# Kernel tuning notes

Hardware: AMD Instinct MI355X
Metric: run time of the kernel (lower is better)

Reference implementation:

```python
import jax, jax.numpy as jnp
import numpy as np

R = 6            # search radius
P = 2 * R + 1    # patch size = 13
D = 4            # mask downsample rate
TOPK = 36        # top-k over patch dim (eval path)


def _corr(fq, fm):
    """Local correlation volume (SpatialCorrelationSampler, kernel=1, patch=P).
    fq, fm: [b,c,h,w] -> [b, P*P, h*w]."""
    b, c, h, w = fq.shape
    fmp = jnp.pad(fm, ((0, 0), (0, 0), (R, R), (R, R)))
    rows = []
    for di in range(P):
        for dj in range(P):
            rows.append(jnp.einsum('bchw,bchw->bhw', fq, fmp[:, :, di:di + h, dj:dj + w]))
    return jnp.stack(rows, 1).reshape(b, P * P, h * w)


def _unfold(msk):
    """F.unfold(msk, kernel_size=P, padding=R): [b,o,h,w] -> [b,o,P*P,h*w]."""
    b, o, h, w = msk.shape
    mp = jnp.pad(msk, ((0, 0), (0, 0), (R, R), (R, R)))
    pats = [mp[:, :, di:di + h, dj:dj + w] for di in range(P) for dj in range(P)]
    return jnp.stack(pats, 2).reshape(b, o, P * P, h * w)


def _forward(feat_query, feat_mem0, feat_mem1, msk_mem0, msk_mem1):
    b, c, h, w = feat_query.shape
    # correlation volumes for each memory frame, concat over patch dim
    corr = jnp.concatenate([_corr(feat_query, feat_mem0),
                            _corr(feat_query, feat_mem1)], axis=1)
    corr = corr / jnp.sqrt(jnp.asarray(c, corr.dtype))          # [b, 2*P*P, N]
    # eval path: top-k over the (frames*P*P) patch axis, per pixel
    corr_t = corr.transpose(0, 2, 1)                              # [b, N, 2PP]
    vals, idx = jax.lax.top_k(corr_t, TOPK)                       # [b, N, K]
    wts = jax.nn.softmax(vals, axis=-1)                           # [b, N, K]
    # downsample masks by strided slicing, unfold, concat over patch dim
    msk = jnp.concatenate([_unfold(msk_mem0[:, :, ::D, ::D]),
                           _unfold(msk_mem1[:, :, ::D, ::D])], axis=2)  # [b,o,2PP,N]
    msk_t = msk.transpose(0, 3, 1, 2)                             # [b, N, o, 2PP]
    g = jnp.take_along_axis(msk_t, idx[:, :, None, :], axis=3)    # [b, N, o, K]
    out = (wts[:, :, None, :] * g).sum(-1)                        # [b, N, o]
    obj = msk_mem0.shape[1]
    return out.transpose(0, 2, 1).reshape(b, obj, h, w)


def setup_inputs() -> dict:
    key = jax.random.key(0)
    k = jax.random.split(key, 5)
    b, c, h, w = 1, 256, 120, 216
    obj = 11
    return {
        'feat_query': jax.random.normal(k[0], (b, c, h, w), jnp.float32),
        'feat_mem0': jax.random.normal(k[1], (b, c, h, w), jnp.float32),
        'feat_mem1': jax.random.normal(k[2], (b, c, h, w), jnp.float32),
        'msk_mem0': jax.random.uniform(k[3], (b, obj, h * D, w * D), jnp.float32),
        'msk_mem1': jax.random.uniform(k[4], (b, obj, h * D, w * D), jnp.float32),
    }


def reference(feat_query, feat_mem0, feat_mem1, msk_mem0, msk_mem1):
    return _forward(feat_query, feat_mem0, feat_mem1, msk_mem0, msk_mem1)
```

## Files before the change

kernel.cpp:

```cpp
#include <hip/hip_runtime.h>
#include <hip/hip_bf16.h>
#include <math.h>

#define H 120
#define W 216
#define C 256
#define NPIX (H*W)
#define PATCH 13
#define PP 169
#define RAD 6
#define TOPKN 36
#define OBJ 11
#define MD 4
#define CW 344

typedef unsigned short ushort;
typedef unsigned int   uint;
typedef __attribute__((ext_vector_type(8))) __bf16 bf16x8;
typedef __attribute__((ext_vector_type(4))) float   f32x4;

#define PLANE_B ((size_t)NPIX * 512)

#define YT 8
#define RT 20
#define XT 16
#define UW 32
#define PXS 128
#define ROWS (UW * PXS)
#define BUFB (RT * ROWS)
#define NXT 14
#define NYT 15
#define NWG (NXT * 2 * NYT)

__device__ inline ushort f2bf_rne(float x) {
  uint u = __float_as_uint(x);
  uint r = (u + 0x7FFFu + ((u >> 16) & 1u)) >> 16;
  return (ushort)r;
}
__device__ inline float bf2f(ushort h) { return __uint_as_float(((uint)h) << 16); }

__global__ __launch_bounds__(256) void k_prep(const float* __restrict__ fq,
                      const float* __restrict__ fm0, const float* __restrict__ fm1,
                      char* fqt, char* fm0t, char* fm1t) {
  const float* src = (blockIdx.z == 0) ? fq : (blockIdx.z == 1) ? fm0 : fm1;
  char* dst = (blockIdx.z == 0) ? fqt : (blockIdx.z == 1) ? fm0t : fm1t;

  const int p0 = blockIdx.x * 64;
  const int c0 = blockIdx.y * 64;
  const int tid = threadIdx.x;

  __shared__ float ts[64 * 65];
  {
    int p = tid & 63, cl = tid >> 6;
    #pragma unroll
    for (int jj = 0; jj < 16; ++jj) {
      int c = 4 * jj + cl;
      ts[c * 65 + p] = src[(size_t)(c0 + c) * NPIX + p0 + p];
    }
  }
  __syncthreads();
  {
    int pl = tid >> 2, sub = tid & 3;
    ushort hb[16], lb[16];
    #pragma unroll
    for (int i = 0; i < 16; ++i) {
      float x = ts[(sub * 16 + i) * 65 + pl];
      ushort h = f2bf_rne(x);
      hb[i] = h;
      lb[i] = f2bf_rne(x - bf2f(h));
    }
    size_t off = (size_t)(p0 + pl) * 512 + (size_t)c0 * 2 + sub * 32;
    *(uint4*)(dst + off)            = ((uint4*)hb)[0];
    *(uint4*)(dst + off + 16)       = ((uint4*)hb)[1];
    *(uint4*)(dst + PLANE_B + off)      = ((uint4*)lb)[0];
    *(uint4*)(dst + PLANE_B + off + 16) = ((uint4*)lb)[1];
  }
}

__global__ void k_downsample(const float* __restrict__ m0, const float* __restrict__ m1,
                             float* __restrict__ mds) {
  int i = blockIdx.x * 256 + threadIdx.x;
  const int total = 2 * OBJ * NPIX;
  if (i >= total) return;
  int fo = i / NPIX;
  int pix = i - fo * NPIX;
  int f = fo / OBJ, o = fo - f * OBJ;
  int y = pix / W, x = pix - y * W;
  const float* src = f ? m1 : m0;
  mds[i] = src[(size_t)o * (H*MD) * (W*MD) + (size_t)(MD*y) * (W*MD) + MD*x];
}

__global__ __launch_bounds__(512, 2) void k_corr_mfma(const char* __restrict__ fqt,
                        const char* __restrict__ fm0t, const char* __restrict__ fm1t,
                        float* __restrict__ corr) {
  int b = blockIdx.x;
  int xcd = b & 7;
  int wgid = ((xcd < 4) ? xcd * 53 : 4 * 53 + (xcd - 4) * 52) + (b >> 3);
  int yt   = wgid % NYT;
  int rest = wgid / NYT;
  int f    = rest & 1;
  int xt   = rest >> 1;

  const int y0 = yt * YT;
  const int X0 = xt * XT;
  const int tid  = threadIdx.x;
  const int wy   = tid >> 6;
  const int lane = tid & 63;
  const int l15  = lane & 15, l4 = lane >> 4;
  const int y    = y0 + wy;

  const char* frame = f ? fm1t : fm0t;

  __shared__ __align__(16) char bsm[2 * BUFB];

  const char* gsrc[10];
  #pragma unroll
  for (int i = 0; i < 10; ++i) {
    int gdest = wy * 640 + i * 64 + lane;
    int ri  = gdest >> 8;
    int rem = gdest & 255;
    int px  = rem >> 3;
    int pqp = rem & 7;
    int pqs = pqp ^ (px & 7);
    int p   = pqs >> 2, q = pqs & 3;
    int r = y0 - 6 + ri;  r = (r < 0) ? 0 : (r >= H ? H - 1 : r);
    int u = X0 - 8 + px;  u = (u < 0) ? 0 : (u >= W ? W - 1 : u);
    gsrc[i] = frame + (size_t)p * PLANE_B + (size_t)(r * W + u) * 512 + q * 16;
  }

  int xA = X0 + l15;
  const char* pa = fqt + (size_t)(y * W + (xA < W ? xA : W - 1)) * 512 + l4 * 16;
  bf16x8 Ah[8], Al[8];
  #pragma unroll
  for (int kc = 0; kc < 8; ++kc) {
    Ah[kc] = *(const bf16x8*)(pa + kc * 64);
    Al[kc] = *(const bf16x8*)(pa + PLANE_B + kc * 64);
  }

  const int px0 = l15, px1 = 16 + l15;
  const uint sw  = (uint)((l15 & 7) << 4);
  const uint b0h = (uint)((px0 * PXS +      l4 * 16) ^ sw);
  const uint b0l = (uint)((px0 * PXS + 64 + l4 * 16) ^ sw);
  const uint b1h = (uint)((px1 * PXS +      l4 * 16) ^ sw);
  const uint b1l = (uint)((px1 * PXS + 64 + l4 * 16) ^ sw);

  int u0 = X0 + l15 - 8;
  int u1 = u0 + 16;
  bool uok0 = (u0 >= 0) && (u0 < W);
  bool uok1 = (u1 >= 0) && (u1 < W);

  f32x4 acc[13][2];
  #pragma unroll
  for (int di = 0; di < 13; ++di) {
    acc[di][0] = (f32x4){0.f, 0.f, 0.f, 0.f};
    acc[di][1] = (f32x4){0.f, 0.f, 0.f, 0.f};
  }

  auto STAGE = [&](int buf, int kc) {
    #pragma unroll
    for (int i = 0; i < 10; ++i)
      __builtin_amdgcn_global_load_lds(
        (const __attribute__((address_space(1))) void*)(gsrc[i] + kc * 64),
        (__attribute__((address_space(3))) void*)(bsm + buf * BUFB + wy * 10240 + i * 1024),
        16, 0, 0);
  };

  STAGE(0, 0);
  __syncthreads();

  #pragma unroll
  for (int kc = 0; kc < 8; ++kc) {
    if (kc < 7) STAGE((kc + 1) & 1, kc + 1);
    const char* bb = bsm + (kc & 1) * BUFB;

    #pragma unroll
    for (int di = 0; di < 13; ++di) {
      int rr = y + di - RAD;
      if (rr >= 0 && rr < H) {
        const char* rb = bb + (wy + di) * ROWS;
        {
          bf16x8 Bhv = *(const bf16x8*)(rb + b0h);
          bf16x8 Blv = *(const bf16x8*)(rb + b0l);
          acc[di][0] = __builtin_amdgcn_mfma_f32_16x16x32_bf16(Ah[kc], Bhv, acc[di][0], 0, 0, 0);
          acc[di][0] = __builtin_amdgcn_mfma_f32_16x16x32_bf16(Ah[kc], Blv, acc[di][0], 0, 0, 0);
          acc[di][0] = __builtin_amdgcn_mfma_f32_16x16x32_bf16(Al[kc], Bhv, acc[di][0], 0, 0, 0);
        }
        {
          bf16x8 Bhv = *(const bf16x8*)(rb + b1h);
          bf16x8 Blv = *(const bf16x8*)(rb + b1l);
          acc[di][1] = __builtin_amdgcn_mfma_f32_16x16x32_bf16(Ah[kc], Bhv, acc[di][1], 0, 0, 0);
          acc[di][1] = __builtin_amdgcn_mfma_f32_16x16x32_bf16(Ah[kc], Blv, acc[di][1], 0, 0, 0);
          acc[di][1] = __builtin_amdgcn_mfma_f32_16x16x32_bf16(Al[kc], Bhv, acc[di][1], 0, 0, 0);
        }
      }
    }
    __syncthreads();
  }

  float* cb = corr + (size_t)(y * W) * CW + f * PP;
  #pragma unroll
  for (int di = 0; di < 13; ++di) {
    #pragma unroll
    for (int nt = 0; nt < 2; ++nt) {
      bool uok = nt ? uok1 : uok0;
      #pragma unroll
      for (int j = 0; j < 4; ++j) {
        int m  = l4 * 4 + j;
        int x  = X0 + m;
        int dj = 16 * nt + l15 - m - 2;
        if (x < W && dj >= 0 && dj < PATCH)
          cb[(size_t)x * CW + di * PATCH + dj] = uok ? acc[di][nt][j] * 0.0625f : 0.f;
      }
    }
  }
}

__global__ __launch_bounds__(64) void k_corr_valu(const float* __restrict__ fq,
                       const float* __restrict__ fm0, const float* __restrict__ fm1,
                       float* __restrict__ corr) {
  int b = blockIdx.x;
  int lb = (b & 7) * 390 + (b >> 3);
  int y   = lb / 26;
  int r26 = lb - y * 26;
  int f   = r26 / 13;
  int di  = r26 - f * 13;
  const int tid = threadIdx.x;
  const int xg  = tid;
  const int r   = y + di - RAD;

  float* corr_base = corr + (size_t)(y * W) * CW + (f * PP + di * PATCH);

  if (r < 0 || r >= H) {
    if (xg < 54) {
      float* cp = corr_base + (size_t)(4 * xg) * CW;
      #pragma unroll
      for (int sub = 0; sub < 4; ++sub) {
        #pragma unroll
        for (int dj = 0; dj < PATCH; ++dj) cp[(size_t)sub * CW + dj] = 0.f;
      }
    }
    return;
  }

  const float* fm = f ? fm1 : fm0;
  __shared__ float fm_s[4 * 232];

  const float* pf[4];
  int  ldsoff[4];
  bool sval[4], mval[4];
  #pragma unroll
  for (int s = 0; s < 4; ++s) {
    int i = tid + 64 * s;
    sval[s] = (i < 232);
    int ii = sval[s] ? i : 0;
    int ch = ii / 58;
    int m  = ii - ch * 58;
    int x  = 4 * m - 8;
    mval[s] = sval[s] && (m >= 2) && (m <= 55);
    ldsoff[s] = ch * 232 + 4 * m;
    pf[s] = fm + (size_t)ch * NPIX + (size_t)r * W + (mval[s] ? x : 0);
  }

  const float* pq = fq + (size_t)y * W + 4 * ((xg < 54) ? xg : 0);

  float4 acc[PATCH];
  #pragma unroll
  for (int d = 0; d < PATCH; ++d) acc[d] = make_float4(0.f, 0.f, 0.f, 0.f);

  for (int c0 = 0; c0 < C; c0 += 4) {
    #pragma unroll
    for (int s = 0; s < 4; ++s) {
      if (sval[s]) {
        float4 v = make_float4(0.f, 0.f, 0.f, 0.f);
        if (mval[s]) v = *(const float4*)(pf[s]);
        *(float4*)&fm_s[ldsoff[s]] = v;
        pf[s] += 4 * (size_t)NPIX;
      }
    }
    __syncthreads();
    if (xg < 54) {
      #pragma unroll
      for (int ch = 0; ch < 4; ++ch) {
        float4 q4 = *(const float4*)(pq + (size_t)ch * NPIX);
        float rv[20];
        #pragma unroll
        for (int qq = 0; qq < 5; ++qq) {
          float4 t4 = *(const float4*)&fm_s[ch * 232 + 4 * xg + 4 * qq];
          rv[4*qq+0] = t4.x; rv[4*qq+1] = t4.y; rv[4*qq+2] = t4.z; rv[4*qq+3] = t4.w;
        }
        #pragma unroll
        for (int dj = 0; dj < PATCH; ++dj) {
          acc[dj].x += q4.x * rv[dj + 2];
          acc[dj].y += q4.y * rv[dj + 3];
          acc[dj].z += q4.z * rv[dj + 4];
          acc[dj].w += q4.w * rv[dj + 5];
        }
      }
      pq += 4 * (size_t)NPIX;
    }
    __syncthreads();
  }

  if (xg < 54) {
    float* cp = corr_base + (size_t)(4 * xg) * CW;
    #pragma unroll
    for (int dj = 0; dj < PATCH; ++dj) {
      cp[dj]                  = acc[dj].x * 0.0625f;
      cp[(size_t)1 * CW + dj] = acc[dj].y * 0.0625f;
      cp[(size_t)2 * CW + dj] = acc[dj].z * 0.0625f;
      cp[(size_t)3 * CW + dj] = acc[dj].w * 0.0625f;
    }
  }
}

__global__ __launch_bounds__(256) void k_topk(const float* __restrict__ corr,
                       const float* __restrict__ mds, float* __restrict__ out) {
  int wid = (blockIdx.x * 256 + threadIdx.x) >> 6;
  int lane = threadIdx.x & 63;
  if (wid >= NPIX) return;
  const float* cr = corr + (size_t)wid * CW;

  float v[6]; uint ui[6];
  #pragma unroll
  for (int s = 0; s < 6; ++s) {
    int idx = lane + 64 * s;
    bool ok = idx < 2 * PP;
    float f = ok ? cr[idx] : 0.f;
    v[s] = f;
    uint bb = __float_as_uint(f);
    uint u = bb ^ (uint)(((int)bb >> 31) | 0x80000000);
    ui[s] = ok ? u : 0u;
  }

  uint blo = 0u, bhi = 0xFFFFFFFFu;
  for (int it = 0; it < 32; ++it) {
    uint mid = blo + ((bhi - blo) >> 1);
    int c = 0;
    #pragma unroll
    for (int s = 0; s < 6; ++s)
      c += __popcll(__ballot(ui[s] > mid));
    if (c <= 35) bhi = mid; else blo = mid + 1;
  }
  const uint x0 = blo;

  int c_gt = 0;
  #pragma unroll
  for (int s = 0; s < 6; ++s) c_gt += __popcll(__ballot(ui[s] > x0));
  const int need = 36 - c_gt;

  uint tb = (x0 & 0x80000000u) ? (x0 ^ 0x80000000u) : ~x0;
  const float tf = __uint_as_float(tb);

  float w[6];
  float zp = 0.f;
  int prior = 0;
  #pragma unroll
  for (int s = 0; s < 6; ++s) {
    unsigned long long tie = __ballot(ui[s] == x0);
    uint below = __builtin_amdgcn_mbcnt_hi((uint)(tie >> 32),
                  __builtin_amdgcn_mbcnt_lo((uint)tie, 0u));
    bool acc = (ui[s] > x0) || ((ui[s] == x0) && ((prior + (int)below) < need));
    prior += __popcll(tie);
    w[s] = acc ? __expf(v[s] - tf) : 0.f;
    zp += w[s];
  }
  float Z = zp;
  #pragma unroll
  for (int off = 32; off >= 1; off >>= 1) Z += __shfl_xor(Z, off, 64);

  int y = wid / W, x = wid - (wid / W) * W;
  float no[OBJ];
  #pragma unroll
  for (int o = 0; o < OBJ; ++o) no[o] = 0.f;
  #pragma unroll
  for (int s = 0; s < 6; ++s) {
    if (w[s] > 0.f) {
      int idx = lane + 64 * s;
      int ff = idx >= PP;
      int r = idx - ff * PP;
      int di = r / PATCH, dj = r - (r / PATCH) * PATCH;
      int yy = y + di - RAD, xx = x + dj - RAD;
      if (yy >= 0 && yy < H && xx >= 0 && xx < W) {
        const float* mb = mds + ((size_t)ff * OBJ) * NPIX + yy * W + xx;
        #pragma unroll
        for (int o = 0; o < OBJ; ++o) no[o] += w[s] * mb[(size_t)o * NPIX];
      }
    }
  }
  float inv = 1.f / Z;
  #pragma unroll
  for (int o = 0; o < OBJ; ++o) {
    float p = no[o];
    #pragma unroll
    for (int off = 32; off >= 1; off >>= 1) p += __shfl_xor(p, off, 64);
    if (lane == 0) out[(size_t)o * NPIX + wid] = p * inv;
  }
}

extern "C" void kernel_launch(void* const* d_in, const int* in_sizes, int n_in,
                              void* d_out, int out_size, void* d_ws, size_t ws_size,
                              hipStream_t stream) {
  const float* fq  = (const float*)d_in[0];
  const float* fm0 = (const float*)d_in[1];
  const float* fm1 = (const float*)d_in[2];
  const float* m0  = (const float*)d_in[3];
  const float* m1  = (const float*)d_in[4];
  float* out = (float*)d_out;

  char* ws = (char*)d_ws;
  size_t off = 0;
  auto alloc = [&](size_t sz) { size_t o = off; off = (off + sz + 1023) & ~(size_t)1023; return o; };

  size_t mds_o  = alloc((size_t)2 * OBJ * NPIX * sizeof(float));
  size_t corr_o = alloc((size_t)NPIX * CW * sizeof(float));
  size_t fqt_o  = alloc(2 * PLANE_B);
  size_t fm0t_o = alloc(2 * PLANE_B);
  size_t fm1t_o = alloc(2 * PLANE_B);
  size_t needed = off;

  float* mds  = (float*)(ws + mds_o);
  float* corr = (float*)(ws + corr_o);

  k_downsample<<<(2 * OBJ * NPIX + 255) / 256, 256, 0, stream>>>(m0, m1, mds);

  if (ws_size >= needed) {
    char* fqt  = ws + fqt_o;
    char* fm0t = ws + fm0t_o;
    char* fm1t = ws + fm1t_o;
    dim3 gp(405, 4, 3);
    k_prep<<<gp, 256, 0, stream>>>(fq, fm0, fm1, fqt, fm0t, fm1t);
    k_corr_mfma<<<NWG, 512, 0, stream>>>(fqt, fm0t, fm1t, corr);
  } else {
    k_corr_valu<<<120 * 26, 64, 0, stream>>>(fq, fm0, fm1, corr);
  }

  k_topk<<<NPIX / 4, 256, 0, stream>>>(corr, mds, out);
}
```

Baseline: 138.5 us.

## Split MFMA corr work across twice the waves and stream A fragments per k-chunk

The correlation kernel now runs 1024 threads per block, with each wave handling a single 16-pixel column tile instead of two. This halves the accumulator registers per wave. The query A fragments are no longer all preloaded; they are loaded per k-chunk with a one-step-ahead prefetch. The aim is to cut VGPR pressure and raise the number of resident waves, so LDS reads and MFMA latency overlap better. In exchange, each wave issues more duplicated A loads, LDS B reads are no longer shared across the two column tiles, and the launch-bounds target of 1024x4 may cause spilling.

```diff
diff --git a/kernel.cpp b/kernel.cpp
--- a/kernel.cpp
+++ b/kernel.cpp
@@ -90,7 +90,7 @@
   mds[i] = src[(size_t)o * (H*MD) * (W*MD) + (size_t)(MD*y) * (W*MD) + MD*x];
 }
 
-__global__ __launch_bounds__(512, 2) void k_corr_mfma(const char* __restrict__ fqt,
+__global__ __launch_bounds__(1024, 4) void k_corr_mfma(const char* __restrict__ fqt,
                         const char* __restrict__ fm0t, const char* __restrict__ fm1t,
                         float* __restrict__ corr) {
   int b = blockIdx.x;
@@ -104,19 +104,21 @@
   const int y0 = yt * YT;
   const int X0 = xt * XT;
   const int tid  = threadIdx.x;
-  const int wy   = tid >> 6;
+  const int wv   = tid >> 6;
+  const int wyy  = wv >> 1;
+  const int nt   = wv & 1;
   const int lane = tid & 63;
   const int l15  = lane & 15, l4 = lane >> 4;
-  const int y    = y0 + wy;
+  const int y    = y0 + wyy;
 
   const char* frame = f ? fm1t : fm0t;
 
   __shared__ __align__(16) char bsm[2 * BUFB];
 
-  const char* gsrc[10];
-  #pragma unroll
-  for (int i = 0; i < 10; ++i) {
-    int gdest = wy * 640 + i * 64 + lane;
+  const char* gsrc[5];
+  #pragma unroll
+  for (int i = 0; i < 5; ++i) {
+    int gdest = wv * 64 + lane + 1024 * i;
     int ri  = gdest >> 8;
     int rem = gdest & 255;
     int px  = rem >> 3;
@@ -130,70 +132,58 @@
 
   int xA = X0 + l15;
   const char* pa = fqt + (size_t)(y * W + (xA < W ? xA : W - 1)) * 512 + l4 * 16;
-  bf16x8 Ah[8], Al[8];
-  #pragma unroll
-  for (int kc = 0; kc < 8; ++kc) {
-    Ah[kc] = *(const bf16x8*)(pa + kc * 64);
-    Al[kc] = *(const bf16x8*)(pa + PLANE_B + kc * 64);
-  }
-
-  const int px0 = l15, px1 = 16 + l15;
+
+  const int pxn = 16 * nt + l15;
   const uint sw  = (uint)((l15 & 7) << 4);
-  const uint b0h = (uint)((px0 * PXS +      l4 * 16) ^ sw);
-  const uint b0l = (uint)((px0 * PXS + 64 + l4 * 16) ^ sw);
-  const uint b1h = (uint)((px1 * PXS +      l4 * 16) ^ sw);
-  const uint b1l = (uint)((px1 * PXS + 64 + l4 * 16) ^ sw);
-
-  int u0 = X0 + l15 - 8;
-  int u1 = u0 + 16;
-  bool uok0 = (u0 >= 0) && (u0 < W);
-  bool uok1 = (u1 >= 0) && (u1 < W);
-
-  f32x4 acc[13][2];
-  #pragma unroll
-  for (int di = 0; di < 13; ++di) {
-    acc[di][0] = (f32x4){0.f, 0.f, 0.f, 0.f};
-    acc[di][1] = (f32x4){0.f, 0.f, 0.f, 0.f};
-  }
+  const uint bh_off = (uint)((pxn * PXS +      l4 * 16) ^ sw);
+  const uint bl_off = (uint)((pxn * PXS + 64 + l4 * 16) ^ sw);
+
+  int u0 = X0 + 16 * nt + l15 - 8;
+  bool uok = (u0 >= 0) && (u0 < W);
+
+  f32x4 acc[13];
+  #pragma unroll
+  for (int di = 0; di < 13; ++di) acc[di] = (f32x4){0.f, 0.f, 0.f, 0.f};
 
   auto STAGE = [&](int buf, int kc) {
     #pragma unroll
-    for (int i = 0; i < 10; ++i)
+    for (int i = 0; i < 5; ++i)
       __builtin_amdgcn_global_load_lds(
         (const __attribute__((address_space(1))) void*)(gsrc[i] + kc * 64),
-        (__attribute__((address_space(3))) void*)(bsm + buf * BUFB + wy * 10240 + i * 1024),
+        (__attribute__((address_space(3))) void*)(bsm + buf * BUFB + wv * 1024 + i * 16384),
         16, 0, 0);
   };
 
   STAGE(0, 0);
+  uint4 aCh = *(const uint4*)(pa);
+  uint4 aCl = *(const uint4*)(pa + PLANE_B);
+  uint4 aNh, aNl;
   __syncthreads();
 
   #pragma unroll
   for (int kc = 0; kc < 8; ++kc) {
-    if (kc < 7) STAGE((kc + 1) & 1, kc + 1);
+    if (kc < 7) {
+      STAGE((kc + 1) & 1, kc + 1);
+      aNh = *(const uint4*)(pa + (kc + 1) * 64);
+      aNl = *(const uint4*)(pa + PLANE_B + (kc + 1) * 64);
+    }
     const char* bb = bsm + (kc & 1) * BUFB;
+    bf16x8 Ahv = __builtin_bit_cast(bf16x8, aCh);
+    bf16x8 Alv = __builtin_bit_cast(bf16x8, aCl);
 
     #pragma unroll
     for (int di = 0; di < 13; ++di) {
       int rr = y + di - RAD;
       if (rr >= 0 && rr < H) {
-        const char* rb = bb + (wy + di) * ROWS;
-        {
-          bf16x8 Bhv = *(const bf16x8*)(rb + b0h);
-          bf16x8 Blv = *(const bf16x8*)(rb + b0l);
-          acc[di][0] = __builtin_amdgcn_mfma_f32_16x16x32_bf16(Ah[kc], Bhv, acc[di][0], 0, 0, 0);
-          acc[di][0] = __builtin_amdgcn_mfma_f32_16x16x32_bf16(Ah[kc], Blv, acc[di][0], 0, 0, 0);
-          acc[di][0] = __builtin_amdgcn_mfma_f32_16x16x32_bf16(Al[kc], Bhv, acc[di][0], 0, 0, 0);
-        }
-        {
-          bf16x8 Bhv = *(const bf16x8*)(rb + b1h);
-          bf16x8 Blv = *(const bf16x8*)(rb + b1l);
-          acc[di][1] = __builtin_amdgcn_mfma_f32_16x16x32_bf16(Ah[kc], Bhv, acc[di][1], 0, 0, 0);
-          acc[di][1] = __builtin_amdgcn_mfma_f32_16x16x32_bf16(Ah[kc], Blv, acc[di][1], 0, 0, 0);
-          acc[di][1] = __builtin_amdgcn_mfma_f32_16x16x32_bf16(Al[kc], Bhv, acc[di][1], 0, 0, 0);
-        }
+        const char* rb = bb + (wyy + di) * ROWS;
+        bf16x8 Bhv = *(const bf16x8*)(rb + bh_off);
+        bf16x8 Blv = *(const bf16x8*)(rb + bl_off);
+        acc[di] = __builtin_amdgcn_mfma_f32_16x16x32_bf16(Ahv, Bhv, acc[di], 0, 0, 0);
+        acc[di] = __builtin_amdgcn_mfma_f32_16x16x32_bf16(Ahv, Blv, acc[di], 0, 0, 0);
+        acc[di] = __builtin_amdgcn_mfma_f32_16x16x32_bf16(Alv, Bhv, acc[di], 0, 0, 0);
       }
     }
+    aCh = aNh; aCl = aNl;
     __syncthreads();
   }
 
@@ -201,16 +191,12 @@
   #pragma unroll
   for (int di = 0; di < 13; ++di) {
     #pragma unroll
-    for (int nt = 0; nt < 2; ++nt) {
-      bool uok = nt ? uok1 : uok0;
-      #pragma unroll
-      for (int j = 0; j < 4; ++j) {
-        int m  = l4 * 4 + j;
-        int x  = X0 + m;
-        int dj = 16 * nt + l15 - m - 2;
-        if (x < W && dj >= 0 && dj < PATCH)
-          cb[(size_t)x * CW + di * PATCH + dj] = uok ? acc[di][nt][j] * 0.0625f : 0.f;
-      }
+    for (int j = 0; j < 4; ++j) {
+      int m  = l4 * 4 + j;
+      int x  = X0 + m;
+      int dj = 16 * nt + l15 - m - 2;
+      if (x < W && dj >= 0 && dj < PATCH)
+        cb[(size_t)x * CW + di * PATCH + dj] = uok ? acc[di][j] * 0.0625f : 0.f;
     }
   }
 }
@@ -429,7 +415,7 @@
     char* fm1t = ws + fm1t_o;
     dim3 gp(405, 4, 3);
     k_prep<<<gp, 256, 0, stream>>>(fq, fm0, fm1, fqt, fm0t, fm1t);
-    k_corr_mfma<<<NWG, 512, 0, stream>>>(fqt, fm0t, fm1t, corr);
+    k_corr_mfma<<<NWG, 1024, 0, stream>>>(fqt, fm0t, fm1t, corr);
   } else {
     k_corr_valu<<<120 * 26, 64, 0, stream>>>(fq, fm0, fm1, corr);
   }
```

After: 134.1 us. -3.2%, faster.
